# Optimization experiments

Hardware: AMD Instinct MI355X
Metric: run time of the kernel (lower is better)

## Reference

```python
import jax, jax.numpy as jnp
import numpy as np

T, B, IN, OUT = 128, 32, 128, 128
N, M, R, H = 256, 64, 4, 256  # mem_slot, mem_size, read_heads, nn_output_size


def setup_inputs() -> dict:
    key = jax.random.key(0)
    ks = jax.random.split(key, 10)
    s = 0.05
    return {
        "xs": jax.random.normal(ks[0], (T, B, IN), jnp.float32),
        "mem0": jax.random.normal(ks[1], (B, N, M), jnp.float32) * s,
        "W_lstm": jax.random.normal(ks[2], (IN + M * R + H, 4 * H), jnp.float32) * s,
        "b_lstm": jnp.zeros((4 * H,), jnp.float32),
        "W_pre": jax.random.normal(ks[3], (H, OUT), jnp.float32) * s,
        "b_pre": jnp.zeros((OUT,), jnp.float32),
        "W_key": jax.random.normal(ks[4], (H, M), jnp.float32) * s,
        "W_beta": jax.random.normal(ks[5], (H, 1), jnp.float32) * s,
        "W_teach": jax.random.normal(ks[6], (H, M), jnp.float32) * s,
        "W_ro": jax.random.normal(ks[7], (M * R, OUT), jnp.float32) * s,
    }


def reference(xs, mem0, W_lstm, b_lstm, W_pre, b_pre, W_key, W_beta, W_teach, W_ro):
    eps = 1e-8

    def step(carry, x):
        mem, h, c, read_vecs, loss = carry
        # controller: LSTM cell over [x, flattened read vectors]
        inp = jnp.concatenate([x, read_vecs.reshape(B, M * R)], axis=-1)
        z = jnp.concatenate([inp, h], axis=-1) @ W_lstm + b_lstm
        i, f, g, o = jnp.split(z, 4, axis=-1)
        c = jax.nn.sigmoid(f) * c + jax.nn.sigmoid(i) * jnp.tanh(g)
        h = jax.nn.sigmoid(o) * jnp.tanh(c)
        pre_out = h @ W_pre + b_pre          # (B, OUT)
        k = h @ W_key                        # (B, M) content key
        beta = jax.nn.softplus(h @ W_beta)   # (B, 1) sharpness
        teacher = h @ W_teach                # (B, M) generated teacher vec
        # cosine similarity between each memory slot and the key
        num = jnp.einsum('bnm,bm->bn', mem, k)
        den = jnp.maximum(
            jnp.linalg.norm(mem, axis=-1) * jnp.linalg.norm(k, axis=-1, keepdims=True), eps)
        sim = num / den                      # (B, N)
        write_w = jax.nn.softmax(beta * sim, axis=-1)  # safe_softmax over slots
        # additive content write (outer product of write weights and key)
        mem = mem + write_w[:, :, None] * k[:, None, :]
        # supervision loss: match generated teacher to written content
        loss = loss + jnp.mean((k - teacher) ** 2)
        # read: write_w broadcast over R heads -> identical reads per head
        read = jnp.einsum('bn,bnm->bm', write_w, mem)  # (B, M)
        read_vecs = jnp.broadcast_to(read[:, :, None], (B, M, R))
        out = pre_out + read_vecs.reshape(B, M * R) @ W_ro
        return (mem, h, c, read_vecs, loss), out

    carry0 = (mem0,
              jnp.zeros((B, H), xs.dtype),
              jnp.zeros((B, H), xs.dtype),
              jnp.zeros((B, M, R), xs.dtype),
              jnp.zeros((), xs.dtype))
    (_, _, _, _, sup_loss), ys = jax.lax.scan(step, carry0, xs)
    return ys, sup_loss
```

## Files before the change

### kernel.cpp

```cpp
#include <hip/hip_runtime.h>

typedef unsigned short u16;
typedef unsigned int u32;
typedef unsigned long long u64;
typedef short short8 __attribute__((ext_vector_type(8)));
typedef float f32x4 __attribute__((ext_vector_type(4)));

__device__ __forceinline__ float b2f(u16 u) {
    unsigned x = ((unsigned)u) << 16;
    return __builtin_bit_cast(float, x);
}
__device__ __forceinline__ u16 f2b(float f) {
    unsigned u = __builtin_bit_cast(unsigned, f);
    u += 0x7FFFu + ((u >> 16) & 1u);
    return (u16)(u >> 16);
}
__device__ __forceinline__ float sigm(float x) { return 1.f / (1.f + __expf(-x)); }
__device__ __forceinline__ float tanh_(float x) { return 1.f - 2.f / (__expf(2.f * x) + 1.f); }

__device__ __forceinline__ u64 lda(const u64* p) {
    return __hip_atomic_load(p, __ATOMIC_RELAXED, __HIP_MEMORY_SCOPE_AGENT);
}
__device__ __forceinline__ void sta(u64* p, u64 v) {
    __hip_atomic_store(p, v, __ATOMIC_RELAXED, __HIP_MEMORY_SCOPE_AGENT);
}
__device__ __forceinline__ unsigned ld_flag(const unsigned* p) {
    return __hip_atomic_load(p, __ATOMIC_RELAXED, __HIP_MEMORY_SCOPE_AGENT);
}
__device__ __forceinline__ void st_flag(unsigned* p, unsigned v) {
    __hip_atomic_store(p, v, __ATOMIC_RELAXED, __HIP_MEMORY_SCOPE_AGENT);
}
__device__ __forceinline__ void ld16x4_issue(const void* p0, const void* p1, const void* p2,
                                             const void* p3, uint4& a, uint4& b, uint4& c, uint4& d) {
    asm volatile(
        "global_load_dwordx4 %0, %4, off sc0 sc1\n\t"
        "global_load_dwordx4 %1, %5, off sc0 sc1\n\t"
        "global_load_dwordx4 %2, %6, off sc0 sc1\n\t"
        "global_load_dwordx4 %3, %7, off sc0 sc1"
        : "=v"(a), "=v"(b), "=v"(c), "=v"(d)
        : "v"(p0), "v"(p1), "v"(p2), "v"(p3) : "memory");
}
__device__ __forceinline__ void wait_vm0() {
    asm volatile("s_waitcnt vmcnt(0)" ::: "memory");
}
__device__ __forceinline__ void st16(void* p, uint4 v) {
    u64 lo = ((u64)v.y << 32) | (u64)v.x;
    u64 hi = ((u64)v.w << 32) | (u64)v.z;
    __hip_atomic_store((u64*)p,     lo, __ATOMIC_RELAXED, __HIP_MEMORY_SCOPE_AGENT);
    __hip_atomic_store((u64*)p + 1, hi, __ATOMIC_RELAXED, __HIP_MEMORY_SCOPE_AGENT);
}

#define T_STEPS 128
#define BATCH   32
#define KHR     320
#define PADK    328
#define MEMPAD  68
#define WKPAD   264

#define WS_BAR      0
#define WS_LOSS     128
#define WS_FLAG     160
#define WS_RT       192
#define WS_HRG      16576
#define WS_ZSET     41088
#define WS_XSF      41216
#define WS_MEM0F    2138368
#define WS_WLF      4235520
#define WS_BLF      6856960
#define WS_WPREF    6861056
#define WS_BPREF    6992128
#define WS_WKEYF    6992640
#define WS_WBETAF   7058176
#define WS_WTEACHF  7059200
#define WS_WROF     7124736
#define WS_XW       7255808
#define WS_WREFF    24033024
#define WS_WKT      24295168
#define WS_WROEFF   24360704
#define WS_HS       24393472
#define WS_RS       28587776

#define HR_OFF   0
#define WF_OFF   20992
#define WK_OFF   41472
#define MEM_OFF  75264
#define Z_OFF    144896
#define C_OFF    149504
#define KV_OFF   151552
#define KP_OFF   152832
#define RP_OFF   153856
#define BR_OFF   154880
#define WR_OFF   154944
#define SC_OFF   155008
#define WB_OFF   155072
#define HST_OFF  156096
#define RST_OFF  156608
#define LDS_TOTAL 156736

__device__ __forceinline__ void gridbar(unsigned* flags, unsigned phase, int rank) {
    __syncthreads();
    if (threadIdx.x < 64) {
        if (threadIdx.x == 0) st_flag(flags + rank, phase);
        long guard = 0;
        for (;;) {
            unsigned v = ld_flag(flags + (threadIdx.x & 31));
            if (__ballot(v < phase) == 0ull) break;
            if (++guard > 1000000L) break;
            if (guard > 4) __builtin_amdgcn_s_sleep(1);
        }
    }
    __syncthreads();
}

__global__ void dnc_normalize(const void* s0, const void* s1, const void* s2, const void* s3,
                              const void* s4, const void* s5, const void* s6, const void* s7,
                              const void* s8, const void* s9, char* __restrict__ ws) {
    __shared__ int cnt;
    if (threadIdx.x == 0) cnt = 0;
    __syncthreads();
    {
        const u16* xs_u16 = (const u16*)s0;
        int c = 0;
        for (int i = threadIdx.x; i < 1024; i += 256) {
            int e = (xs_u16[i] >> 7) & 0xFF;
            if (e >= 96 && e <= 135) c++;
        }
        atomicAdd(&cnt, c);
    }
    __syncthreads();
    const int bf = (cnt > 820) ? 1 : 0;
    if (blockIdx.x == 0 && threadIdx.x == 0) *(int*)(ws + WS_FLAG) = bf;
    const void* srcs[10] = {s0, s1, s2, s3, s4, s5, s6, s7, s8, s9};
    const int sizes[10] = {524288, 524288, 655360, 1024, 32768, 128, 16384, 256, 16384, 32768};
    const int bases[10] = {WS_XSF, WS_MEM0F, WS_WLF, WS_BLF, WS_WPREF, WS_BPREF,
                           WS_WKEYF, WS_WBETAF, WS_WTEACHF, WS_WROF};
    const int gt = blockIdx.x * 256 + threadIdx.x, gs = gridDim.x * 256;
    for (int s = 0; s < 10; ++s) {
        float* dst = (float*)(ws + bases[s]);
        const int n = sizes[s];
        if (bf) {
            const u16* p = (const u16*)srcs[s];
            for (int i = gt; i < n; i += gs) dst[i] = b2f(p[i]);
        } else {
            const float* p = (const float*)srcs[s];
            for (int i = gt; i < n; i += gs) dst[i] = p[i];
        }
    }
}

__global__ void dnc_prologue(char* __restrict__ ws) {
    extern __shared__ float xls[];
    const float* XSF     = (const float*)(ws + WS_XSF);
    const float* WLF     = (const float*)(ws + WS_WLF);
    const float* BLF     = (const float*)(ws + WS_BLF);
    const float* WKEYF   = (const float*)(ws + WS_WKEYF);
    const float* WTEACHF = (const float*)(ws + WS_WTEACHF);
    const float* WROF    = (const float*)(ws + WS_WROF);
    float* xW  = (float*)(ws + WS_XW);
    float* WrE = (float*)(ws + WS_WREFF);
    float* Wkt = (float*)(ws + WS_WKT);
    float* Wre = (float*)(ws + WS_WROEFF);
    const int wg = blockIdx.x, tid = threadIdx.x;
    if (wg < 512) {
        const int rb = wg >> 4, cb = wg & 15;
        const float4* xsrc = (const float4*)(XSF + (size_t)rb * 16384);
        for (int i = tid; i < 4096; i += 256) {
            float4 v = xsrc[i];
            int row = i >> 5, c4 = (i & 31) * 4;
            float* d = xls + row * 129 + c4;
            d[0] = v.x; d[1] = v.y; d[2] = v.z; d[3] = v.w;
        }
        __syncthreads();
        const int tr = tid >> 4, tc = tid & 15;
        const int c0 = cb * 64 + tc * 4;
        float acc[8][4];
#pragma unroll
        for (int rr = 0; rr < 8; ++rr) {
            acc[rr][0] = BLF[c0]; acc[rr][1] = BLF[c0 + 1];
            acc[rr][2] = BLF[c0 + 2]; acc[rr][3] = BLF[c0 + 3];
        }
        for (int k = 0; k < 128; ++k) {
            float4 w4 = *(const float4*)(WLF + (size_t)k * 1024 + c0);
#pragma unroll
            for (int rr = 0; rr < 8; ++rr) {
                float xv = xls[(tr * 8 + rr) * 129 + k];
                acc[rr][0] += xv * w4.x; acc[rr][1] += xv * w4.y;
                acc[rr][2] += xv * w4.z; acc[rr][3] += xv * w4.w;
            }
        }
#pragma unroll
        for (int rr = 0; rr < 8; ++rr) {
            size_t o = (size_t)(rb * 128 + tr * 8 + rr) * 1024 + c0;
            *(float4*)(xW + o) = make_float4(acc[rr][0], acc[rr][1], acc[rr][2], acc[rr][3]);
        }
    } else if (wg < 576) {
        const int m = wg - 512;
        const int c = tid * 4;
#pragma unroll
        for (int e = 0; e < 4; ++e) {
            float s = 0.f;
#pragma unroll
            for (int rr = 0; rr < 4; ++rr) s += WLF[(size_t)(128 + 4 * m + rr) * 1024 + c + e];
            WrE[m * 1024 + c + e] = s;
        }
    } else if (wg < 592) {
        const int i = (wg - 576) * 1024 + tid * 4;
#pragma unroll
        for (int e = 0; e < 4; ++e) Wkt[i + e] = WKEYF[i + e] - WTEACHF[i + e];
    } else if (wg < 600) {
        const int i = (wg - 592) * 1024 + tid * 4;
#pragma unroll
        for (int e = 0; e < 4; ++e) {
            int m = (i + e) >> 7, c = (i + e) & 127;
            float s = 0.f;
#pragma unroll
            for (int rr = 0; rr < 4; ++rr) s += WROF[(4 * m + rr) * 128 + c];
            Wre[i + e] = s;
        }
    }
}

__global__ __launch_bounds__(256, 1) void dnc_main(char* __restrict__ ws) {
    extern __shared__ char smem[];
    u16*   hr_lds = (u16*)(smem + HR_OFF);
    u16*   wfrag  = (u16*)(smem + WF_OFF);
    u16*   wkeyT  = (u16*)(smem + WK_OFF);
    float* memA   = (float*)(smem + MEM_OFF);
    float* z_lds  = (float*)(smem + Z_OFF);
    float* c_lds  = (float*)(smem + C_OFF);
    float* kv     = (float*)(smem + KV_OFF);
    float* kpart  = (float*)(smem + KP_OFF);
    float* rp     = (float*)(smem + RP_OFF);
    float* bred   = (float*)(smem + BR_OFF);
    float* wred   = (float*)(smem + WR_OFF);
    float* sc     = (float*)(smem + SC_OFF);
    float* wbF    = (float*)(smem + WB_OFF);
    u16*   hstage = (u16*)(smem + HST_OFF);
    u16*   rstage = (u16*)(smem + RST_OFF);

    const int tid  = threadIdx.x;
    const int wg   = blockIdx.x;
    const int lane = tid & 63;
    const int wid  = tid >> 6;

    unsigned* flags = (unsigned*)(ws + WS_BAR);
    u64* rT         = (u64*)(ws + WS_RT);
    u16* hrg        = (u16*)(ws + WS_HRG);
    const float* xWF     = (const float*)(ws + WS_XW);
    const float* WrEffF  = (const float*)(ws + WS_WREFF);
    const float* WLF     = (const float*)(ws + WS_WLF);
    const float* WKEYF   = (const float*)(ws + WS_WKEYF);
    const float* WBETAF  = (const float*)(ws + WS_WBETAF);
    const float* MEM0F   = (const float*)(ws + WS_MEM0F);
    float* HsF = (float*)(ws + WS_HS);
    float* RsF = (float*)(ws + WS_RS);

    for (int i = tid; i < 32 * PADK; i += 256) hr_lds[i] = 0;
    for (int idx = tid; idx < 10240; idx += 256) {
        int k = idx >> 5, c = idx & 31;
        int kt = k >> 5, q = (k >> 3) & 3, j = k & 7;
        int gcol = (c >> 3) * 256 + wg * 8 + (c & 7);
        float v = (k < 64) ? WrEffF[k * 1024 + gcol]
                           : WLF[(size_t)(384 + (k - 64)) * 1024 + gcol];
        wfrag[((kt * 4 + q) * 32 + c) * 8 + j] = f2b(v);
    }
    for (int i = tid; i < 256 * 64; i += 256) {
        int k = i >> 6, m = i & 63;
        wkeyT[m * WKPAD + k] = f2b(WKEYF[i]);
    }
    wbF[tid]   = WBETAF[tid];
    c_lds[tid] = 0.f;
    for (int i = tid; i < 256 * 64; i += 256) {
        int n = i >> 6, m = i & 63;
        memA[n * MEMPAD + m] = MEM0F[wg * 16384 + i];
    }
    __syncthreads();

    const int bt = wid & 1, ct = wid >> 1;
    const int fm = lane & 15, fq = lane >> 4;
    const int pb = tid >> 3, pu = tid & 7;

    float xg0, xg1, xg2, xg3;
    {
        const size_t xb = (size_t)pb * 1024 + wg * 8 + pu;
        xg0 = xWF[xb]; xg1 = xWF[xb + 256]; xg2 = xWF[xb + 512]; xg3 = xWF[xb + 768];
    }
    f32x4 hWacc = {0.f, 0.f, 0.f, 0.f};

    for (int t = 0; t < T_STEPS; ++t) {
        {
            const u64* rch = rT + (size_t)((((t + 1) & 1) * 32 + pb) * 16 + 2 * pu) * 2;
            const u32 want = (u32)t;
            u64 v0, v1, v2, v3;
            long guard = 0;
            for (;;) {
                v0 = lda(rch); v1 = lda(rch + 1); v2 = lda(rch + 2); v3 = lda(rch + 3);
                bool ok = ((u32)v0 == want) && ((u32)(v1 >> 32) == want) &&
                          ((u32)v2 == want) && ((u32)(v3 >> 32) == want);
                if (ok) break;
                if (++guard > 2000000L) break;
                if (guard > 4) __builtin_amdgcn_s_sleep(1);
            }
            u32* dst = (u32*)hr_lds + pb * 164 + 4 * pu;
            dst[0] = (u32)(v0 >> 32); dst[1] = (u32)v1;
            dst[2] = (u32)(v2 >> 32); dst[3] = (u32)v3;
        }
        __syncthreads();

        f32x4 acc = hWacc;
#pragma unroll
        for (int kt = 0; kt < 2; ++kt) {
            short8 a = *(const short8*)(hr_lds + (bt * 16 + fm) * PADK + kt * 32 + fq * 8);
            short8 b = *(const short8*)(wfrag + ((kt * 4 + fq) * 32 + ct * 16 + fm) * 8);
            acc = __builtin_amdgcn_mfma_f32_16x16x32_bf16(a, b, acc, 0, 0, 0);
        }
#pragma unroll
        for (int r = 0; r < 4; ++r) {
            int bb = bt * 16 + fq * 4 + r;
            int cc = ct * 16 + fm;
            z_lds[bb * 36 + cc] = acc[r];
        }
        __syncthreads();

        {
            float iv = z_lds[pb * 36 + pu]      + xg0;
            float fv = z_lds[pb * 36 + 8 + pu]  + xg1;
            float gv = z_lds[pb * 36 + 16 + pu] + xg2;
            float ov = z_lds[pb * 36 + 24 + pu] + xg3;
            float co = c_lds[pb * 8 + pu];
            float cn = sigm(fv) * co + sigm(iv) * tanh_(gv);
            float hn = sigm(ov) * tanh_(cn);
            c_lds[pb * 8 + pu] = cn;
            hstage[pb * 8 + pu] = f2b(hn);
            HsF[(size_t)(t * BATCH + pb) * 256 + wg * 8 + pu] = hn;
        }
        __syncthreads();
        if (tid < 32) {
            uint4 hv = *(const uint4*)(hstage + tid * 8);
            st16(hrg + tid * KHR + 64 + wg * 8, hv);
        }
        gridbar(flags, (unsigned)(t + 1), wg);

        uint4 ha, hb4, hc, hd;
        {
            const u16* src = hrg + pb * KHR + 64 + pu * 32;
            ld16x4_issue(src, src + 8, src + 16, src + 24, ha, hb4, hc, hd);
        }
        {
            int tn = (t + 1 < T_STEPS) ? t + 1 : 127;
            const size_t xb = (size_t)(tn * BATCH + pb) * 1024 + wg * 8 + pu;
            xg0 = xWF[xb]; xg1 = xWF[xb + 256]; xg2 = xWF[xb + 512]; xg3 = xWF[xb + 768];
        }
        float nr2 = 0.f;
        {
            const float4* mrow = (const float4*)(memA + tid * MEMPAD);
#pragma unroll
            for (int i = 0; i < 16; ++i) {
                float4 m4 = mrow[i];
                nr2 += m4.x * m4.x + m4.y * m4.y + m4.z * m4.z + m4.w * m4.w;
            }
        }
        wait_vm0();
        {
            u16* dst = hr_lds + pb * PADK + 64 + pu * 32;
            *(uint4*)(dst)      = ha;
            *(uint4*)(dst + 8)  = hb4;
            *(uint4*)(dst + 16) = hc;
            *(uint4*)(dst + 24) = hd;
        }
        __syncthreads();

        {
            f32x4 hz = {0.f, 0.f, 0.f, 0.f};
#pragma unroll
            for (int kt = 2; kt < 10; ++kt) {
                short8 a = *(const short8*)(hr_lds + (bt * 16 + fm) * PADK + kt * 32 + fq * 8);
                short8 b = *(const short8*)(wfrag + ((kt * 4 + fq) * 32 + ct * 16 + fm) * 8);
                hz = __builtin_amdgcn_mfma_f32_16x16x32_bf16(a, b, hz, 0, 0, 0);
            }
            hWacc = hz;
        }

        const u16* hrow = hr_lds + wg * PADK + 64;
        {
            float a = 0.f;
#pragma unroll
            for (int i = 0; i < 8; ++i) {
                short8 w8 = *(const short8*)(wkeyT + lane * WKPAD + wid * 64 + i * 8);
                short8 h8 = *(const short8*)(hrow + wid * 64 + i * 8);
#pragma unroll
                for (int e = 0; e < 8; ++e)
                    a += b2f((u16)h8[e]) * b2f((u16)w8[e]);
            }
            kpart[wid * 64 + lane] = a;
        }
        {
            float bp = b2f(hrow[tid]) * wbF[tid];
#pragma unroll
            for (int off = 32; off > 0; off >>= 1) bp += __shfl_xor(bp, off, 64);
            if (lane == 0) bred[wid] = bp;
        }
        __syncthreads();
        if (tid < 64) {
            float kk = kpart[tid] + kpart[64 + tid] + kpart[128 + tid] + kpart[192 + tid];
            kv[tid] = kk;
            float k2 = kk * kk;
#pragma unroll
            for (int off = 32; off > 0; off >>= 1) k2 += __shfl_xor(k2, off, 64);
            if (tid == 0) sc[1] = sqrtf(k2);
        } else if (tid == 64) {
            float zb = bred[0] + bred[1] + bred[2] + bred[3];
            sc[0] = logf(1.f + __expf(zb));
        }
        __syncthreads();
        const float beta = sc[0], knorm = sc[1];

        float num = 0.f;
        {
            const float4* mrow = (const float4*)(memA + tid * MEMPAD);
            const float4* k4p  = (const float4*)kv;
#pragma unroll
            for (int i = 0; i < 16; ++i) {
                float4 m4 = mrow[i], k4 = k4p[i];
                num += m4.x * k4.x + m4.y * k4.y + m4.z * k4.z + m4.w * k4.w;
            }
        }
        float den = fmaxf(sqrtf(nr2) * knorm, 1e-8f);
        float s   = beta * (num / den);
        float wm = s;
#pragma unroll
        for (int off = 32; off > 0; off >>= 1) wm = fmaxf(wm, __shfl_xor(wm, off, 64));
        float ev = __expf(s - wm);
        float wsum = ev, wsumsq = ev * ev;
#pragma unroll
        for (int off = 32; off > 0; off >>= 1) {
            wsum   += __shfl_xor(wsum, off, 64);
            wsumsq += __shfl_xor(wsumsq, off, 64);
        }
        if (lane == 0) { wred[wid] = wm; wred[4 + wid] = wsum; wred[8 + wid] = wsumsq; }
        __syncthreads();
        float gm = fmaxf(fmaxf(wred[0], wred[1]), fmaxf(wred[2], wred[3]));
        float e0 = __expf(wred[0] - gm), e1 = __expf(wred[1] - gm);
        float e2 = __expf(wred[2] - gm), e3 = __expf(wred[3] - gm);
        float gsum  = wred[4] * e0 + wred[5] * e1 + wred[6] * e2 + wred[7] * e3;
        float gsumq = wred[8] * e0 * e0 + wred[9] * e1 * e1
                    + wred[10] * e2 * e2 + wred[11] * e3 * e3;
        float w   = __expf(s - gm) / gsum;
        float wsq = gsumq / (gsum * gsum);

        {
            const int lm = lane & 15, q = lane >> 4;
            float r0 = 0.f, r1 = 0.f, r2 = 0.f, r3 = 0.f;
#pragma unroll
            for (int i = 0; i < 16; ++i) {
                float wn = __shfl(w, i * 4 + q, 64);
                float4 m4 = *(const float4*)(memA + (wid * 64 + i * 4 + q) * MEMPAD + 4 * lm);
                r0 += wn * m4.x; r1 += wn * m4.y; r2 += wn * m4.z; r3 += wn * m4.w;
            }
            r0 += __shfl_xor(r0, 16, 64); r0 += __shfl_xor(r0, 32, 64);
            r1 += __shfl_xor(r1, 16, 64); r1 += __shfl_xor(r1, 32, 64);
            r2 += __shfl_xor(r2, 16, 64); r2 += __shfl_xor(r2, 32, 64);
            r3 += __shfl_xor(r3, 16, 64); r3 += __shfl_xor(r3, 32, 64);
            if (q == 0) {
                rp[wid * 64 + 4 * lm + 0] = r0;
                rp[wid * 64 + 4 * lm + 1] = r1;
                rp[wid * 64 + 4 * lm + 2] = r2;
                rp[wid * 64 + 4 * lm + 3] = r3;
            }
        }
        __syncthreads();
        if (tid < 64) {
            float rd = rp[tid] + rp[64 + tid] + rp[128 + tid] + rp[192 + tid]
                     + wsq * kv[tid];
            rstage[tid] = f2b(rd);
            RsF[(size_t)(t * BATCH + wg) * 64 + tid] = rd;
        }
        __syncthreads();
        if (tid < 16) {
            const u32* rs32 = (const u32*)rstage;
            u32 w0 = rs32[2 * tid], w1 = rs32[2 * tid + 1];
            u64* dstc = rT + (size_t)(((t & 1) * 32 + wg) * 16 + tid) * 2;
            const u64 tag = (u64)(u32)(t + 1);
            sta(dstc,     ((u64)w0 << 32) | tag);
            sta(dstc + 1, (tag << 32) | w1);
        }
        {
            const int lm = lane & 15, q = lane >> 4;
            float4 k4 = ((const float4*)kv)[lm];
#pragma unroll
            for (int i = 0; i < 16; ++i) {
                float wn = __shfl(w, i * 4 + q, 64);
                float4* mp = (float4*)(memA + (wid * 64 + i * 4 + q) * MEMPAD + 4 * lm);
                float4 m4 = *mp;
                m4.x += wn * k4.x; m4.y += wn * k4.y; m4.z += wn * k4.z; m4.w += wn * k4.w;
                *mp = m4;
            }
        }
    }
}

__global__ void dnc_epilogue(char* __restrict__ ws, void* __restrict__ outv) {
    __shared__ float hs8[8][256];
    __shared__ float rs8[8][64];
    __shared__ float lacc;
    const float* HsF   = (const float*)(ws + WS_HS);
    const float* RsF   = (const float*)(ws + WS_RS);
    const float* WktF  = (const float*)(ws + WS_WKT);
    const float* WreF  = (const float*)(ws + WS_WROEFF);
    const float* WpreF = (const float*)(ws + WS_WPREF);
    const float* bpreF = (const float*)(ws + WS_BPREF);
    float* lossacc = (float*)(ws + WS_LOSS);
    const int bf = *(const int*)(ws + WS_FLAG);
    const int tid = threadIdx.x;
    const size_t r0 = (size_t)blockIdx.x * 8;
    if (tid == 0) lacc = 0.f;
    for (int i = tid; i < 8 * 256; i += 256) hs8[i >> 8][i & 255] = HsF[r0 * 256 + i];
    for (int i = tid; i < 8 * 64; i += 256)  rs8[i >> 6][i & 63]  = RsF[r0 * 64 + i];
    __syncthreads();
    {
        const int rl = tid >> 5, c0 = (tid & 31) * 4;
        float a0 = bpreF[c0], a1 = bpreF[c0 + 1], a2 = bpreF[c0 + 2], a3 = bpreF[c0 + 3];
        for (int k = 0; k < 256; ++k) {
            float hv = hs8[rl][k];
            float4 w4 = *(const float4*)(WpreF + k * 128 + c0);
            a0 += hv * w4.x; a1 += hv * w4.y; a2 += hv * w4.z; a3 += hv * w4.w;
        }
        for (int m = 0; m < 64; ++m) {
            float rv = rs8[rl][m];
            float4 w4 = *(const float4*)(WreF + m * 128 + c0);
            a0 += rv * w4.x; a1 += rv * w4.y; a2 += rv * w4.z; a3 += rv * w4.w;
        }
        size_t o = (r0 + rl) * 128 + c0;
        if (bf) {
            u16* out = (u16*)outv;
            out[o] = f2b(a0); out[o + 1] = f2b(a1); out[o + 2] = f2b(a2); out[o + 3] = f2b(a3);
        } else {
            float* out = (float*)outv;
            out[o] = a0; out[o + 1] = a1; out[o + 2] = a2; out[o + 3] = a3;
        }
    }
    {
        const int rl = tid >> 5, m0 = (tid & 31) * 2;
        float d0 = 0.f, d1 = 0.f;
        for (int k = 0; k < 256; ++k) {
            float hv = hs8[rl][k];
            d0 += hv * WktF[k * 64 + m0];
            d1 += hv * WktF[k * 64 + m0 + 1];
        }
        float p = d0 * d0 + d1 * d1;
#pragma unroll
        for (int off = 32; off > 0; off >>= 1) p += __shfl_xor(p, off, 64);
        if ((tid & 63) == 0) atomicAdd(&lacc, p);
        __syncthreads();
        if (tid == 0) atomicAdd(lossacc, lacc);
    }
}

__global__ void dnc_loss_fin(const char* __restrict__ ws, void* __restrict__ outv) {
    if (threadIdx.x == 0 && blockIdx.x == 0) {
        float l = *(const float*)(ws + WS_LOSS) * (1.f / 2048.f);
        if (*(const int*)(ws + WS_FLAG)) ((u16*)outv)[524288] = f2b(l);
        else                             ((float*)outv)[524288] = l;
    }
}

extern "C" void kernel_launch(void* const* d_in, const int* in_sizes, int n_in,
                              void* d_out, int out_size, void* d_ws, size_t ws_size,
                              hipStream_t stream) {
    char* ws = (char*)d_ws;
    hipMemsetAsync(d_ws, 0, WS_ZSET, stream);
    dnc_normalize<<<512, 256, 0, stream>>>(d_in[0], d_in[1], d_in[2], d_in[3], d_in[4],
                                           d_in[5], d_in[6], d_in[7], d_in[8], d_in[9], ws);
    (void)hipFuncSetAttribute((const void*)dnc_prologue,
                              hipFuncAttributeMaxDynamicSharedMemorySize, 128 * 129 * 4);
    dnc_prologue<<<600, 256, 128 * 129 * 4, stream>>>(ws);
    (void)hipFuncSetAttribute((const void*)dnc_main,
                              hipFuncAttributeMaxDynamicSharedMemorySize, LDS_TOTAL);
    dnc_main<<<32, 256, LDS_TOTAL, stream>>>(ws);
    dnc_epilogue<<<512, 256, 0, stream>>>(ws, d_out);
    dnc_loss_fin<<<1, 64, 0, stream>>>(ws, d_out);
}
```

Baseline: 1.040 ms.

## Fuse epilogue into persistent main kernel as flag-driven consumer blocks

Launches 256 blocks of the main kernel. The first 32 run the recurrent scan, and the other 224 poll per-step barrier flags to compute outputs and the loss for finished timesteps while the scan continues. This overlaps the epilogue with the serial recurrence and drops one kernel launch. It also stores the precomputed input projection xW as bf16 to halve its traffic, keeps the LSTM cell state in registers, and replaces the LDS staging of h and r with wave shuffles and direct stores. Risks include consumer blocks competing for CUs and memory bandwidth with the scan, spin-wait cost, and the precision loss from bf16 xW.

```diff
diff --git a/kernel.cpp b/kernel.cpp
--- a/kernel.cpp
+++ b/kernel.cpp
@@ -15,6 +15,8 @@
     u += 0x7FFFu + ((u >> 16) & 1u);
     return (u16)(u >> 16);
 }
+__device__ __forceinline__ float lo16f(u32 u) { return __builtin_bit_cast(float, u << 16); }
+__device__ __forceinline__ float hi16f(u32 u) { return __builtin_bit_cast(float, u & 0xFFFF0000u); }
 __device__ __forceinline__ float sigm(float x) { return 1.f / (1.f + __expf(-x)); }
 __device__ __forceinline__ float tanh_(float x) { return 1.f - 2.f / (__expf(2.f * x) + 1.f); }
 
@@ -24,11 +26,20 @@
 __device__ __forceinline__ void sta(u64* p, u64 v) {
     __hip_atomic_store(p, v, __ATOMIC_RELAXED, __HIP_MEMORY_SCOPE_AGENT);
 }
+__device__ __forceinline__ void sta32(u32* p, u32 v) {
+    __hip_atomic_store(p, v, __ATOMIC_RELAXED, __HIP_MEMORY_SCOPE_AGENT);
+}
 __device__ __forceinline__ unsigned ld_flag(const unsigned* p) {
     return __hip_atomic_load(p, __ATOMIC_RELAXED, __HIP_MEMORY_SCOPE_AGENT);
 }
 __device__ __forceinline__ void st_flag(unsigned* p, unsigned v) {
     __hip_atomic_store(p, v, __ATOMIC_RELAXED, __HIP_MEMORY_SCOPE_AGENT);
+}
+__device__ __forceinline__ uint4 ld16c(const void* p) {
+    uint4 v;
+    asm volatile("global_load_dwordx4 %0, %1, off sc0 sc1\n\ts_waitcnt vmcnt(0)"
+                 : "=v"(v) : "v"(p) : "memory");
+    return v;
 }
 __device__ __forceinline__ void ld16x4_issue(const void* p0, const void* p1, const void* p2,
                                              const void* p3, uint4& a, uint4& b, uint4& c, uint4& d) {
@@ -48,6 +59,9 @@
     u64 hi = ((u64)v.w << 32) | (u64)v.z;
     __hip_atomic_store((u64*)p,     lo, __ATOMIC_RELAXED, __HIP_MEMORY_SCOPE_AGENT);
     __hip_atomic_store((u64*)p + 1, hi, __ATOMIC_RELAXED, __HIP_MEMORY_SCOPE_AGENT);
+}
+__device__ __forceinline__ u64 packf2(float a, float b) {
+    return ((u64)__builtin_bit_cast(u32, b) << 32) | (u64)__builtin_bit_cast(u32, a);
 }
 
 #define T_STEPS 128
@@ -85,7 +99,6 @@
 #define WK_OFF   41472
 #define MEM_OFF  75264
 #define Z_OFF    144896
-#define C_OFF    149504
 #define KV_OFF   151552
 #define KP_OFF   152832
 #define RP_OFF   153856
@@ -93,8 +106,6 @@
 #define WR_OFF   154944
 #define SC_OFF   155008
 #define WB_OFF   155072
-#define HST_OFF  156096
-#define RST_OFF  156608
 #define LDS_TOTAL 156736
 
 __device__ __forceinline__ void gridbar(unsigned* flags, unsigned phase, int rank) {
@@ -156,7 +167,7 @@
     const float* WKEYF   = (const float*)(ws + WS_WKEYF);
     const float* WTEACHF = (const float*)(ws + WS_WTEACHF);
     const float* WROF    = (const float*)(ws + WS_WROF);
-    float* xW  = (float*)(ws + WS_XW);
+    u32*   xW  = (u32*)(ws + WS_XW);
     float* WrE = (float*)(ws + WS_WREFF);
     float* Wkt = (float*)(ws + WS_WKT);
     float* Wre = (float*)(ws + WS_WROEFF);
@@ -190,8 +201,10 @@
         }
 #pragma unroll
         for (int rr = 0; rr < 8; ++rr) {
-            size_t o = (size_t)(rb * 128 + tr * 8 + rr) * 1024 + c0;
-            *(float4*)(xW + o) = make_float4(acc[rr][0], acc[rr][1], acc[rr][2], acc[rr][3]);
+            size_t o = (size_t)(rb * 128 + tr * 8 + rr) * 512 + cb * 32 + tc * 2;
+            u32 p0 = (u32)f2b(acc[rr][0]) | ((u32)f2b(acc[rr][1]) << 16);
+            u32 p1 = (u32)f2b(acc[rr][2]) | ((u32)f2b(acc[rr][3]) << 16);
+            *(uint2*)(xW + o) = make_uint2(p0, p1);
         }
     } else if (wg < 576) {
         const int m = wg - 512;
@@ -220,14 +233,87 @@
     }
 }
 
-__global__ __launch_bounds__(256, 1) void dnc_main(char* __restrict__ ws) {
+__global__ __launch_bounds__(256, 1) void dnc_main(char* __restrict__ ws, void* __restrict__ outv) {
     extern __shared__ char smem[];
+    const int tid = threadIdx.x;
+    unsigned* flags = (unsigned*)(ws + WS_BAR);
+
+    if (blockIdx.x >= 32) {
+        float* hs8 = (float*)smem;
+        float* rs8 = (float*)(smem + 8192);
+        float* lacc = (float*)(smem + 10240);
+        const float* WktF  = (const float*)(ws + WS_WKT);
+        const float* WreF  = (const float*)(ws + WS_WROEFF);
+        const float* WpreF = (const float*)(ws + WS_WPREF);
+        const float* bpreF = (const float*)(ws + WS_BPREF);
+        float* lossacc = (float*)(ws + WS_LOSS);
+        const int bf = *(const int*)(ws + WS_FLAG);
+        for (int chunk = (int)blockIdx.x - 32; chunk < 512; chunk += 224) {
+            const int t = chunk >> 2;
+            const unsigned need = (t < 127) ? (unsigned)(t + 2) : 129u;
+            if (tid < 64) {
+                long g = 0;
+                for (;;) {
+                    unsigned v = ld_flag(flags + (tid & 31));
+                    if (__ballot(v < need) == 0ull) break;
+                    if (++g > 30000000L) break;
+                    __builtin_amdgcn_s_sleep(8);
+                }
+            }
+            if (tid == 0) lacc[0] = 0.f;
+            __syncthreads();
+            const size_t r0 = (size_t)chunk * 8;
+            for (int i = tid; i < 512; i += 256)
+                ((uint4*)hs8)[i] = ld16c((const char*)ws + WS_HS + (r0 * 256 + (size_t)i * 4) * 4);
+            if (tid < 128)
+                ((uint4*)rs8)[tid] = ld16c((const char*)ws + WS_RS + (r0 * 64 + (size_t)tid * 4) * 4);
+            __syncthreads();
+            {
+                const int rl = tid >> 5, c0 = (tid & 31) * 4;
+                float a0 = bpreF[c0], a1 = bpreF[c0 + 1], a2 = bpreF[c0 + 2], a3 = bpreF[c0 + 3];
+                for (int k = 0; k < 256; ++k) {
+                    float hv = hs8[rl * 256 + k];
+                    float4 w4 = *(const float4*)(WpreF + k * 128 + c0);
+                    a0 += hv * w4.x; a1 += hv * w4.y; a2 += hv * w4.z; a3 += hv * w4.w;
+                }
+                for (int m = 0; m < 64; ++m) {
+                    float rv = rs8[rl * 64 + m];
+                    float4 w4 = *(const float4*)(WreF + m * 128 + c0);
+                    a0 += rv * w4.x; a1 += rv * w4.y; a2 += rv * w4.z; a3 += rv * w4.w;
+                }
+                size_t o = (r0 + rl) * 128 + c0;
+                if (bf) {
+                    u16* out = (u16*)outv;
+                    out[o] = f2b(a0); out[o + 1] = f2b(a1); out[o + 2] = f2b(a2); out[o + 3] = f2b(a3);
+                } else {
+                    float* out = (float*)outv;
+                    out[o] = a0; out[o + 1] = a1; out[o + 2] = a2; out[o + 3] = a3;
+                }
+            }
+            {
+                const int rl = tid >> 5, m0 = (tid & 31) * 2;
+                float d0 = 0.f, d1 = 0.f;
+                for (int k = 0; k < 256; ++k) {
+                    float hv = hs8[rl * 256 + k];
+                    d0 += hv * WktF[k * 64 + m0];
+                    d1 += hv * WktF[k * 64 + m0 + 1];
+                }
+                float p = d0 * d0 + d1 * d1;
+#pragma unroll
+                for (int off = 32; off > 0; off >>= 1) p += __shfl_xor(p, off, 64);
+                if ((tid & 63) == 0) atomicAdd(lacc, p);
+            }
+            __syncthreads();
+            if (tid == 0) atomicAdd(lossacc, lacc[0]);
+        }
+        return;
+    }
+
     u16*   hr_lds = (u16*)(smem + HR_OFF);
     u16*   wfrag  = (u16*)(smem + WF_OFF);
     u16*   wkeyT  = (u16*)(smem + WK_OFF);
     float* memA   = (float*)(smem + MEM_OFF);
     float* z_lds  = (float*)(smem + Z_OFF);
-    float* c_lds  = (float*)(smem + C_OFF);
     float* kv     = (float*)(smem + KV_OFF);
     float* kpart  = (float*)(smem + KP_OFF);
     float* rp     = (float*)(smem + RP_OFF);
@@ -235,24 +321,20 @@
     float* wred   = (float*)(smem + WR_OFF);
     float* sc     = (float*)(smem + SC_OFF);
     float* wbF    = (float*)(smem + WB_OFF);
-    u16*   hstage = (u16*)(smem + HST_OFF);
-    u16*   rstage = (u16*)(smem + RST_OFF);
-
-    const int tid  = threadIdx.x;
+
     const int wg   = blockIdx.x;
     const int lane = tid & 63;
     const int wid  = tid >> 6;
 
-    unsigned* flags = (unsigned*)(ws + WS_BAR);
-    u64* rT         = (u64*)(ws + WS_RT);
-    u16* hrg        = (u16*)(ws + WS_HRG);
-    const float* xWF     = (const float*)(ws + WS_XW);
+    u64* rT  = (u64*)(ws + WS_RT);
+    u16* hrg = (u16*)(ws + WS_HRG);
+    const u32*   xWP     = (const u32*)(ws + WS_XW);
     const float* WrEffF  = (const float*)(ws + WS_WREFF);
     const float* WLF     = (const float*)(ws + WS_WLF);
     const float* WKEYF   = (const float*)(ws + WS_WKEYF);
     const float* WBETAF  = (const float*)(ws + WS_WBETAF);
     const float* MEM0F   = (const float*)(ws + WS_MEM0F);
-    float* HsF = (float*)(ws + WS_HS);
+    u32* HsA = (u32*)(ws + WS_HS);
     float* RsF = (float*)(ws + WS_RS);
 
     for (int i = tid; i < 32 * PADK; i += 256) hr_lds[i] = 0;
@@ -268,8 +350,7 @@
         int k = i >> 6, m = i & 63;
         wkeyT[m * WKPAD + k] = f2b(WKEYF[i]);
     }
-    wbF[tid]   = WBETAF[tid];
-    c_lds[tid] = 0.f;
+    wbF[tid] = WBETAF[tid];
     for (int i = tid; i < 256 * 64; i += 256) {
         int n = i >> 6, m = i & 63;
         memA[n * MEMPAD + m] = MEM0F[wg * 16384 + i];
@@ -279,11 +360,14 @@
     const int bt = wid & 1, ct = wid >> 1;
     const int fm = lane & 15, fq = lane >> 4;
     const int pb = tid >> 3, pu = tid & 7;
+    float c_reg = 0.f;
 
     float xg0, xg1, xg2, xg3;
     {
-        const size_t xb = (size_t)pb * 1024 + wg * 8 + pu;
-        xg0 = xWF[xb]; xg1 = xWF[xb + 256]; xg2 = xWF[xb + 512]; xg3 = xWF[xb + 768];
+        const size_t xb = (size_t)pb * 512 + wg * 4 + (pu >> 1);
+        u32 u0 = xWP[xb], u1 = xWP[xb + 128], u2 = xWP[xb + 256], u3 = xWP[xb + 384];
+        if (pu & 1) { xg0 = hi16f(u0); xg1 = hi16f(u1); xg2 = hi16f(u2); xg3 = hi16f(u3); }
+        else        { xg0 = lo16f(u0); xg1 = lo16f(u1); xg2 = lo16f(u2); xg3 = lo16f(u3); }
     }
     f32x4 hWacc = {0.f, 0.f, 0.f, 0.f};
 
@@ -322,22 +406,29 @@
         }
         __syncthreads();
 
+        float hn;
         {
             float iv = z_lds[pb * 36 + pu]      + xg0;
             float fv = z_lds[pb * 36 + 8 + pu]  + xg1;
             float gv = z_lds[pb * 36 + 16 + pu] + xg2;
             float ov = z_lds[pb * 36 + 24 + pu] + xg3;
-            float co = c_lds[pb * 8 + pu];
-            float cn = sigm(fv) * co + sigm(iv) * tanh_(gv);
-            float hn = sigm(ov) * tanh_(cn);
-            c_lds[pb * 8 + pu] = cn;
-            hstage[pb * 8 + pu] = f2b(hn);
-            HsF[(size_t)(t * BATCH + pb) * 256 + wg * 8 + pu] = hn;
-        }
-        __syncthreads();
-        if (tid < 32) {
-            uint4 hv = *(const uint4*)(hstage + tid * 8);
-            st16(hrg + tid * KHR + 64 + wg * 8, hv);
+            float cn = sigm(fv) * c_reg + sigm(iv) * tanh_(gv);
+            hn = sigm(ov) * tanh_(cn);
+            c_reg = cn;
+            sta32(HsA + (size_t)(t * BATCH + pb) * 256 + wg * 8 + pu,
+                  __builtin_bit_cast(u32, hn));
+        }
+        {
+            u32 hbits = (u32)f2b(hn);
+            int base = lane & 56;
+            u32 w0 = __shfl(hbits, base + 0, 64) | (__shfl(hbits, base + 1, 64) << 16);
+            u32 w1 = __shfl(hbits, base + 2, 64) | (__shfl(hbits, base + 3, 64) << 16);
+            u32 w2 = __shfl(hbits, base + 4, 64) | (__shfl(hbits, base + 5, 64) << 16);
+            u32 w3 = __shfl(hbits, base + 6, 64) | (__shfl(hbits, base + 7, 64) << 16);
+            if ((lane & 7) == 0) {
+                uint4 hv; hv.x = w0; hv.y = w1; hv.z = w2; hv.w = w3;
+                st16(hrg + pb * KHR + 64 + wg * 8, hv);
+            }
         }
         gridbar(flags, (unsigned)(t + 1), wg);
 
@@ -348,8 +439,10 @@
         }
         {
             int tn = (t + 1 < T_STEPS) ? t + 1 : 127;
-            const size_t xb = (size_t)(tn * BATCH + pb) * 1024 + wg * 8 + pu;
-            xg0 = xWF[xb]; xg1 = xWF[xb + 256]; xg2 = xWF[xb + 512]; xg3 = xWF[xb + 768];
+            const size_t xb = (size_t)(tn * BATCH + pb) * 512 + wg * 4 + (pu >> 1);
+            u32 u0 = xWP[xb], u1 = xWP[xb + 128], u2 = xWP[xb + 256], u3 = xWP[xb + 384];
+            if (pu & 1) { xg0 = hi16f(u0); xg1 = hi16f(u1); xg2 = hi16f(u2); xg3 = hi16f(u3); }
+            else        { xg0 = lo16f(u0); xg1 = lo16f(u1); xg2 = lo16f(u2); xg3 = lo16f(u3); }
         }
         float nr2 = 0.f;
         {
@@ -469,20 +562,20 @@
             }
         }
         __syncthreads();
-        if (tid < 64) {
-            float rd = rp[tid] + rp[64 + tid] + rp[128 + tid] + rp[192 + tid]
-                     + wsq * kv[tid];
-            rstage[tid] = f2b(rd);
-            RsF[(size_t)(t * BATCH + wg) * 64 + tid] = rd;
-        }
-        __syncthreads();
         if (tid < 16) {
-            const u32* rs32 = (const u32*)rstage;
-            u32 w0 = rs32[2 * tid], w1 = rs32[2 * tid + 1];
+            float rd0 = rp[4 * tid]     + rp[64 + 4 * tid]     + rp[128 + 4 * tid]     + rp[192 + 4 * tid]     + wsq * kv[4 * tid];
+            float rd1 = rp[4 * tid + 1] + rp[64 + 4 * tid + 1] + rp[128 + 4 * tid + 1] + rp[192 + 4 * tid + 1] + wsq * kv[4 * tid + 1];
+            float rd2 = rp[4 * tid + 2] + rp[64 + 4 * tid + 2] + rp[128 + 4 * tid + 2] + rp[192 + 4 * tid + 2] + wsq * kv[4 * tid + 2];
+            float rd3 = rp[4 * tid + 3] + rp[64 + 4 * tid + 3] + rp[128 + 4 * tid + 3] + rp[192 + 4 * tid + 3] + wsq * kv[4 * tid + 3];
+            u32 w0 = (u32)f2b(rd0) | ((u32)f2b(rd1) << 16);
+            u32 w1 = (u32)f2b(rd2) | ((u32)f2b(rd3) << 16);
             u64* dstc = rT + (size_t)(((t & 1) * 32 + wg) * 16 + tid) * 2;
             const u64 tag = (u64)(u32)(t + 1);
             sta(dstc,     ((u64)w0 << 32) | tag);
             sta(dstc + 1, (tag << 32) | w1);
+            u64* rdst = (u64*)(RsF + (size_t)(t * BATCH + wg) * 64 + 4 * tid);
+            sta(rdst,     packf2(rd0, rd1));
+            sta(rdst + 1, packf2(rd2, rd3));
         }
         {
             const int lm = lane & 15, q = lane >> 4;
@@ -497,63 +590,8 @@
             }
         }
     }
-}
-
-__global__ void dnc_epilogue(char* __restrict__ ws, void* __restrict__ outv) {
-    __shared__ float hs8[8][256];
-    __shared__ float rs8[8][64];
-    __shared__ float lacc;
-    const float* HsF   = (const float*)(ws + WS_HS);
-    const float* RsF   = (const float*)(ws + WS_RS);
-    const float* WktF  = (const float*)(ws + WS_WKT);
-    const float* WreF  = (const float*)(ws + WS_WROEFF);
-    const float* WpreF = (const float*)(ws + WS_WPREF);
-    const float* bpreF = (const float*)(ws + WS_BPREF);
-    float* lossacc = (float*)(ws + WS_LOSS);
-    const int bf = *(const int*)(ws + WS_FLAG);
-    const int tid = threadIdx.x;
-    const size_t r0 = (size_t)blockIdx.x * 8;
-    if (tid == 0) lacc = 0.f;
-    for (int i = tid; i < 8 * 256; i += 256) hs8[i >> 8][i & 255] = HsF[r0 * 256 + i];
-    for (int i = tid; i < 8 * 64; i += 256)  rs8[i >> 6][i & 63]  = RsF[r0 * 64 + i];
     __syncthreads();
-    {
-        const int rl = tid >> 5, c0 = (tid & 31) * 4;
-        float a0 = bpreF[c0], a1 = bpreF[c0 + 1], a2 = bpreF[c0 + 2], a3 = bpreF[c0 + 3];
-        for (int k = 0; k < 256; ++k) {
-            float hv = hs8[rl][k];
-            float4 w4 = *(const float4*)(WpreF + k * 128 + c0);
-            a0 += hv * w4.x; a1 += hv * w4.y; a2 += hv * w4.z; a3 += hv * w4.w;
-        }
-        for (int m = 0; m < 64; ++m) {
-            float rv = rs8[rl][m];
-            float4 w4 = *(const float4*)(WreF + m * 128 + c0);
-            a0 += rv * w4.x; a1 += rv * w4.y; a2 += rv * w4.z; a3 += rv * w4.w;
-        }
-        size_t o = (r0 + rl) * 128 + c0;
-        if (bf) {
-            u16* out = (u16*)outv;
-            out[o] = f2b(a0); out[o + 1] = f2b(a1); out[o + 2] = f2b(a2); out[o + 3] = f2b(a3);
-        } else {
-            float* out = (float*)outv;
-            out[o] = a0; out[o + 1] = a1; out[o + 2] = a2; out[o + 3] = a3;
-        }
-    }
-    {
-        const int rl = tid >> 5, m0 = (tid & 31) * 2;
-        float d0 = 0.f, d1 = 0.f;
-        for (int k = 0; k < 256; ++k) {
-            float hv = hs8[rl][k];
-            d0 += hv * WktF[k * 64 + m0];
-            d1 += hv * WktF[k * 64 + m0 + 1];
-        }
-        float p = d0 * d0 + d1 * d1;
-#pragma unroll
-        for (int off = 32; off > 0; off >>= 1) p += __shfl_xor(p, off, 64);
-        if ((tid & 63) == 0) atomicAdd(&lacc, p);
-        __syncthreads();
-        if (tid == 0) atomicAdd(lossacc, lacc);
-    }
+    if (tid == 0) st_flag(flags + wg, 129u);
 }
 
 __global__ void dnc_loss_fin(const char* __restrict__ ws, void* __restrict__ outv) {
@@ -576,7 +614,6 @@
     dnc_prologue<<<600, 256, 128 * 129 * 4, stream>>>(ws);
     (void)hipFuncSetAttribute((const void*)dnc_main,
                               hipFuncAttributeMaxDynamicSharedMemorySize, LDS_TOTAL);
-    dnc_main<<<32, 256, LDS_TOTAL, stream>>>(ws);
-    dnc_epilogue<<<512, 256, 0, stream>>>(ws, d_out);
+    dnc_main<<<256, 256, LDS_TOTAL, stream>>>(ws, d_out);
     dnc_loss_fin<<<1, 64, 0, stream>>>(ws, d_out);
 }
```

Result: slower. 1.200 ms (+15.4%).

## Store xW gates in bf16 and drop LDS staging barriers in LSTM step

Applied to the files above, without the earlier changes.

The precomputed input-gate projections xW are now written as packed bf16 instead of fp32, which halves the per-step global reads of x contributions. The LSTM cell state moves from LDS into a register. The h and read vectors are packed with wave shuffles instead of LDS staging, removing two __syncthreads per timestep on the serial critical path. Rounding xW to bf16 adds precision loss in the gate inputs.

```diff
diff --git a/kernel.cpp b/kernel.cpp
--- a/kernel.cpp
+++ b/kernel.cpp
@@ -15,6 +15,8 @@
     u += 0x7FFFu + ((u >> 16) & 1u);
     return (u16)(u >> 16);
 }
+__device__ __forceinline__ float lo16f(u32 u) { return __builtin_bit_cast(float, u << 16); }
+__device__ __forceinline__ float hi16f(u32 u) { return __builtin_bit_cast(float, u & 0xFFFF0000u); }
 __device__ __forceinline__ float sigm(float x) { return 1.f / (1.f + __expf(-x)); }
 __device__ __forceinline__ float tanh_(float x) { return 1.f - 2.f / (__expf(2.f * x) + 1.f); }
 
@@ -85,7 +87,6 @@
 #define WK_OFF   41472
 #define MEM_OFF  75264
 #define Z_OFF    144896
-#define C_OFF    149504
 #define KV_OFF   151552
 #define KP_OFF   152832
 #define RP_OFF   153856
@@ -93,8 +94,6 @@
 #define WR_OFF   154944
 #define SC_OFF   155008
 #define WB_OFF   155072
-#define HST_OFF  156096
-#define RST_OFF  156608
 #define LDS_TOTAL 156736
 
 __device__ __forceinline__ void gridbar(unsigned* flags, unsigned phase, int rank) {
@@ -156,7 +155,7 @@
     const float* WKEYF   = (const float*)(ws + WS_WKEYF);
     const float* WTEACHF = (const float*)(ws + WS_WTEACHF);
     const float* WROF    = (const float*)(ws + WS_WROF);
-    float* xW  = (float*)(ws + WS_XW);
+    u32*   xW  = (u32*)(ws + WS_XW);
     float* WrE = (float*)(ws + WS_WREFF);
     float* Wkt = (float*)(ws + WS_WKT);
     float* Wre = (float*)(ws + WS_WROEFF);
@@ -190,8 +189,10 @@
         }
 #pragma unroll
         for (int rr = 0; rr < 8; ++rr) {
-            size_t o = (size_t)(rb * 128 + tr * 8 + rr) * 1024 + c0;
-            *(float4*)(xW + o) = make_float4(acc[rr][0], acc[rr][1], acc[rr][2], acc[rr][3]);
+            size_t o = (size_t)(rb * 128 + tr * 8 + rr) * 512 + cb * 32 + tc * 2;
+            u32 p0 = (u32)f2b(acc[rr][0]) | ((u32)f2b(acc[rr][1]) << 16);
+            u32 p1 = (u32)f2b(acc[rr][2]) | ((u32)f2b(acc[rr][3]) << 16);
+            *(uint2*)(xW + o) = make_uint2(p0, p1);
         }
     } else if (wg < 576) {
         const int m = wg - 512;
@@ -227,7 +228,6 @@
     u16*   wkeyT  = (u16*)(smem + WK_OFF);
     float* memA   = (float*)(smem + MEM_OFF);
     float* z_lds  = (float*)(smem + Z_OFF);
-    float* c_lds  = (float*)(smem + C_OFF);
     float* kv     = (float*)(smem + KV_OFF);
     float* kpart  = (float*)(smem + KP_OFF);
     float* rp     = (float*)(smem + RP_OFF);
@@ -235,8 +235,6 @@
     float* wred   = (float*)(smem + WR_OFF);
     float* sc     = (float*)(smem + SC_OFF);
     float* wbF    = (float*)(smem + WB_OFF);
-    u16*   hstage = (u16*)(smem + HST_OFF);
-    u16*   rstage = (u16*)(smem + RST_OFF);
 
     const int tid  = threadIdx.x;
     const int wg   = blockIdx.x;
@@ -246,7 +244,7 @@
     unsigned* flags = (unsigned*)(ws + WS_BAR);
     u64* rT         = (u64*)(ws + WS_RT);
     u16* hrg        = (u16*)(ws + WS_HRG);
-    const float* xWF     = (const float*)(ws + WS_XW);
+    const u32*   xWP     = (const u32*)(ws + WS_XW);
     const float* WrEffF  = (const float*)(ws + WS_WREFF);
     const float* WLF     = (const float*)(ws + WS_WLF);
     const float* WKEYF   = (const float*)(ws + WS_WKEYF);
@@ -268,8 +266,7 @@
         int k = i >> 6, m = i & 63;
         wkeyT[m * WKPAD + k] = f2b(WKEYF[i]);
     }
-    wbF[tid]   = WBETAF[tid];
-    c_lds[tid] = 0.f;
+    wbF[tid] = WBETAF[tid];
     for (int i = tid; i < 256 * 64; i += 256) {
         int n = i >> 6, m = i & 63;
         memA[n * MEMPAD + m] = MEM0F[wg * 16384 + i];
@@ -279,11 +276,14 @@
     const int bt = wid & 1, ct = wid >> 1;
     const int fm = lane & 15, fq = lane >> 4;
     const int pb = tid >> 3, pu = tid & 7;
+    float c_reg = 0.f;
 
     float xg0, xg1, xg2, xg3;
     {
-        const size_t xb = (size_t)pb * 1024 + wg * 8 + pu;
-        xg0 = xWF[xb]; xg1 = xWF[xb + 256]; xg2 = xWF[xb + 512]; xg3 = xWF[xb + 768];
+        const size_t xb = (size_t)pb * 512 + wg * 4 + (pu >> 1);
+        u32 u0 = xWP[xb], u1 = xWP[xb + 128], u2 = xWP[xb + 256], u3 = xWP[xb + 384];
+        if (pu & 1) { xg0 = hi16f(u0); xg1 = hi16f(u1); xg2 = hi16f(u2); xg3 = hi16f(u3); }
+        else        { xg0 = lo16f(u0); xg1 = lo16f(u1); xg2 = lo16f(u2); xg3 = lo16f(u3); }
     }
     f32x4 hWacc = {0.f, 0.f, 0.f, 0.f};
 
@@ -322,22 +322,28 @@
         }
         __syncthreads();
 
+        float hn;
         {
             float iv = z_lds[pb * 36 + pu]      + xg0;
             float fv = z_lds[pb * 36 + 8 + pu]  + xg1;
             float gv = z_lds[pb * 36 + 16 + pu] + xg2;
             float ov = z_lds[pb * 36 + 24 + pu] + xg3;
-            float co = c_lds[pb * 8 + pu];
-            float cn = sigm(fv) * co + sigm(iv) * tanh_(gv);
-            float hn = sigm(ov) * tanh_(cn);
-            c_lds[pb * 8 + pu] = cn;
-            hstage[pb * 8 + pu] = f2b(hn);
+            float cn = sigm(fv) * c_reg + sigm(iv) * tanh_(gv);
+            hn = sigm(ov) * tanh_(cn);
+            c_reg = cn;
             HsF[(size_t)(t * BATCH + pb) * 256 + wg * 8 + pu] = hn;
         }
-        __syncthreads();
-        if (tid < 32) {
-            uint4 hv = *(const uint4*)(hstage + tid * 8);
-            st16(hrg + tid * KHR + 64 + wg * 8, hv);
+        {
+            u32 hbits = (u32)f2b(hn);
+            int base = lane & 56;
+            u32 w0 = __shfl(hbits, base + 0, 64) | (__shfl(hbits, base + 1, 64) << 16);
+            u32 w1 = __shfl(hbits, base + 2, 64) | (__shfl(hbits, base + 3, 64) << 16);
+            u32 w2 = __shfl(hbits, base + 4, 64) | (__shfl(hbits, base + 5, 64) << 16);
+            u32 w3 = __shfl(hbits, base + 6, 64) | (__shfl(hbits, base + 7, 64) << 16);
+            if ((lane & 7) == 0) {
+                uint4 hv; hv.x = w0; hv.y = w1; hv.z = w2; hv.w = w3;
+                st16(hrg + pb * KHR + 64 + wg * 8, hv);
+            }
         }
         gridbar(flags, (unsigned)(t + 1), wg);
 
@@ -348,8 +354,10 @@
         }
         {
             int tn = (t + 1 < T_STEPS) ? t + 1 : 127;
-            const size_t xb = (size_t)(tn * BATCH + pb) * 1024 + wg * 8 + pu;
-            xg0 = xWF[xb]; xg1 = xWF[xb + 256]; xg2 = xWF[xb + 512]; xg3 = xWF[xb + 768];
+            const size_t xb = (size_t)(tn * BATCH + pb) * 512 + wg * 4 + (pu >> 1);
+            u32 u0 = xWP[xb], u1 = xWP[xb + 128], u2 = xWP[xb + 256], u3 = xWP[xb + 384];
+            if (pu & 1) { xg0 = hi16f(u0); xg1 = hi16f(u1); xg2 = hi16f(u2); xg3 = hi16f(u3); }
+            else        { xg0 = lo16f(u0); xg1 = lo16f(u1); xg2 = lo16f(u2); xg3 = lo16f(u3); }
         }
         float nr2 = 0.f;
         {
@@ -469,20 +477,19 @@
             }
         }
         __syncthreads();
-        if (tid < 64) {
-            float rd = rp[tid] + rp[64 + tid] + rp[128 + tid] + rp[192 + tid]
-                     + wsq * kv[tid];
-            rstage[tid] = f2b(rd);
-            RsF[(size_t)(t * BATCH + wg) * 64 + tid] = rd;
-        }
-        __syncthreads();
         if (tid < 16) {
-            const u32* rs32 = (const u32*)rstage;
-            u32 w0 = rs32[2 * tid], w1 = rs32[2 * tid + 1];
+            float rd0 = rp[4 * tid]     + rp[64 + 4 * tid]     + rp[128 + 4 * tid]     + rp[192 + 4 * tid]     + wsq * kv[4 * tid];
+            float rd1 = rp[4 * tid + 1] + rp[64 + 4 * tid + 1] + rp[128 + 4 * tid + 1] + rp[192 + 4 * tid + 1] + wsq * kv[4 * tid + 1];
+            float rd2 = rp[4 * tid + 2] + rp[64 + 4 * tid + 2] + rp[128 + 4 * tid + 2] + rp[192 + 4 * tid + 2] + wsq * kv[4 * tid + 2];
+            float rd3 = rp[4 * tid + 3] + rp[64 + 4 * tid + 3] + rp[128 + 4 * tid + 3] + rp[192 + 4 * tid + 3] + wsq * kv[4 * tid + 3];
+            u32 w0 = (u32)f2b(rd0) | ((u32)f2b(rd1) << 16);
+            u32 w1 = (u32)f2b(rd2) | ((u32)f2b(rd3) << 16);
             u64* dstc = rT + (size_t)(((t & 1) * 32 + wg) * 16 + tid) * 2;
             const u64 tag = (u64)(u32)(t + 1);
             sta(dstc,     ((u64)w0 << 32) | tag);
             sta(dstc + 1, (tag << 32) | w1);
+            float* rdst = RsF + (size_t)(t * BATCH + wg) * 64 + 4 * tid;
+            rdst[0] = rd0; rdst[1] = rd1; rdst[2] = rd2; rdst[3] = rd3;
         }
         {
             const int lm = lane & 15, q = lane >> 4;
```

Measured after the change: 1.053 ms. About the same (+1.2%).
